# Performance work log

Measured on AMD Instinct MI355X. Metric: run time of the kernel, lower is better.

The kernel has to match this reference:

```python
import jax, jax.numpy as jnp
import numpy as np

B, T, U = 64, 512, 1024
TIME_STEP = 0.008

# Rieke cone phototransduction parameters (scaleFac = 1, values are final)
PR = dict(sigma=22.0, phi=22.0, eta=2000.0, beta=9.0, cgmp2cur=0.01,
          cgmphill=3.0, cdark=1.0, betaSlow=0.4, hillcoef=4.0,
          hillaffinity=0.5, gamma=10.0, gdark=20.0)


def setup_inputs() -> dict:
    key = jax.random.key(0)
    X = jax.random.uniform(key, (B, T, U), dtype=jnp.float32)  # light intensity >= 0
    inp = {"X_fun": X}
    for name, v in PR.items():
        inp[name] = jnp.full((1, U), v, dtype=jnp.float32)  # flax param shape (1, units)
    return inp


def reference(X_fun, sigma, phi, eta, beta, cgmp2cur, cgmphill, cdark,
              betaSlow, hillcoef, hillaffinity, gamma, gdark):
    # Derived constants (as in runRiekeModel preamble)
    darkCurrent = gdark ** cgmphill * cgmp2cur / 2
    gdark_e = (2 * darkCurrent / cgmp2cur) ** (1 / cgmphill)
    cur2ca = beta * cdark / darkCurrent
    smax = eta / phi * gdark_e * (1 + (cdark / hillaffinity) ** hillcoef)

    Bd, Td, Ud = X_fun.shape
    ones = jnp.ones((Bd, Ud), X_fun.dtype)
    g0 = gdark_e * ones
    s0 = gdark_e * eta / phi * ones
    c0 = cdark * ones
    cslow0 = cdark * ones
    r0 = X_fun[:, 0, :] * gamma / sigma
    p0 = (eta + r0) / phi

    def step(carry, x_prev):
        g, s, c, cslow, p, r = carry
        r_n = r + TIME_STEP * (-sigma * r) + gamma * x_prev
        p_n = p + TIME_STEP * (r + eta - phi * p)
        c_n = c + TIME_STEP * (cur2ca * cgmp2cur * g ** cgmphill
                               / (1 + cslow / cdark) - beta * c)
        cslow_n = cslow - TIME_STEP * (betaSlow * (cslow - c))
        s_n = smax / (1 + (c_n / hillaffinity) ** hillcoef)
        g_n = g + TIME_STEP * (s - p * g)
        return (g_n, s_n, c_n, cslow_n, p_n, r_n), g_n

    xs = jnp.moveaxis(X_fun[:, :-1, :], 1, 0)  # [T-1, B, U], step pnt uses X[:, pnt-1, :]
    _, g_seq = jax.lax.scan(step, (g0, s0, c0, cslow0, p0, r0), xs)
    # g[:, 0, :] stays zero in the original (loop starts at pnt=1)
    g = jnp.concatenate([jnp.zeros((Bd, 1, Ud), X_fun.dtype),
                         jnp.moveaxis(g_seq, 0, 1)], axis=1)
    return -(cgmp2cur * g ** cgmphill) / 2
```

## Files before the change

kernel.cpp:

```cpp
#include <hip/hip_runtime.h>
#include <math.h>


#define TT 512
#define UU 1024
#define DTSTEP 0.008f

__device__ __forceinline__ void gload16(const float* g, float* l) {
    __builtin_amdgcn_global_load_lds(
        (__attribute__((address_space(1))) void*)(uintptr_t)g,
        (__attribute__((address_space(3))) void*)l, 16, 0, 0);
}

__device__ __forceinline__ void run_fast(
    const float* __restrict__ xrow, float* __restrict__ out, unsigned ob,
    const float* gstage, float* __restrict__ wlds, int lane,
    float sigma, float phi, float eta, float beta, float cgmp2cur,
    float cdark, float betaSlow, float hillaff, float gam, float gdark)
{
    const float darkCurrent = gdark * gdark * gdark * cgmp2cur * 0.5f;
    const float gdark_e = gdark;
    const float cur2ca = beta * cdark / darkCurrent;
    const float ha2 = (cdark / hillaff) * (cdark / hillaff);
    const float smax = eta / phi * gdark_e * (1.0f + ha2 * ha2);

    const float Ar   = 1.0f - DTSTEP * sigma;
    const float P1   = 1.0f - DTSTEP * phi;
    const float Ke   = DTSTEP * eta;
    const float icd  = 1.0f / cdark;
    const float KC   = DTSTEP * cur2ca * cgmp2cur;
    const float C1   = 1.0f - DTSTEP * beta;
    const float dtbs = DTSTEP * betaSlow;
    const float iha  = 1.0f / hillaff;
    const float outk = -0.5f * cgmp2cur;

    float g  = gdark_e;
    float s  = gdark_e * eta / phi;
    float c  = cdark;
    float cs = cdark;
    float x0 = xrow[0];
    float r  = x0 * gam / sigma;
    float p  = (eta + r) / phi;
    float gp = g * g * g;

    out[ob - UU] = 0.0f;

#pragma unroll
    for (int j = 0; j < 4; ++j) {
        gload16(gstage, wlds + j * 256);
        gstage += 4 * UU;
    }

    auto step = [&](float x, float& o) {
        float rn  = fmaf(Ar, r, gam * x);
        float pn  = fmaf(P1, p, fmaf(DTSTEP, r, Ke));
        float den = fmaf(cs, icd, 1.0f);
        float rd  = __builtin_amdgcn_rcpf(den);
        float cn  = fmaf(KC, gp * rd, C1 * c);
        float csn = fmaf(-dtbs, cs - c, cs);
        float t2  = cn * iha;
        t2 *= t2;
        float sn  = smax * __builtin_amdgcn_rcpf(fmaf(t2, t2, 1.0f));
        float gn  = fmaf(DTSTEP, fmaf(-p, g, s), g);
        float gpn = gn * gn * gn;
        o = outk * gpn;
        g = gn; s = sn; c = cn; cs = csn; p = pn; r = rn; gp = gpn;
    };

    auto phase = [&](int buf, bool dostage, bool first) {
        if (first) asm volatile("s_waitcnt vmcnt(0)" ::: "memory");
        else       asm volatile("s_waitcnt vmcnt(16)" ::: "memory");
        __builtin_amdgcn_sched_barrier(0);
        if (dostage) {
#pragma unroll
            for (int j = 0; j < 4; ++j) {
                gload16(gstage, wlds + (buf ^ 1) * 1024 + j * 256);
                gstage += 4 * UU;
            }
        }
        __builtin_amdgcn_sched_barrier(0);
        const float* rb = wlds + buf * 1024 + lane;
        float xa[16];
#pragma unroll
        for (int k = 0; k < 16; ++k) xa[k] = rb[k * 64];
        __builtin_amdgcn_sched_barrier(0);
#pragma unroll
        for (int k = 0; k < 16; ++k) {
            float o;
            step(xa[k], o);
            out[ob + (unsigned)(k * UU)] = o;
        }
        ob += 16u * UU;
    };

    phase(0, true, true);
    for (int n2 = 0; n2 < 15; ++n2) {
        phase(1, true, false);
        phase(0, true, false);
    }
    asm volatile("s_waitcnt vmcnt(16)" ::: "memory");
    __builtin_amdgcn_sched_barrier(0);
    {
        const float* rb = wlds + 1024 + lane;
        float xa[16];
#pragma unroll
        for (int k = 0; k < 16; ++k) xa[k] = rb[k * 64];
#pragma unroll
        for (int k = 0; k < 15; ++k) {
            float o;
            step(xa[k], o);
            out[ob + (unsigned)(k * UU)] = o;
        }
    }
}

__device__ void run_generic(
    const float* __restrict__ xrow, float* __restrict__ out, unsigned ob,
    float sigma, float phi, float eta, float beta, float cgmp2cur,
    float cgmphill, float cdark, float betaSlow, float hillcoef,
    float hillaff, float gam, float gdark)
{
    const float darkCurrent = powf(gdark, cgmphill) * cgmp2cur * 0.5f;
    const float gdark_e = powf(2.0f * darkCurrent / cgmp2cur, 1.0f / cgmphill);
    const float cur2ca = beta * cdark / darkCurrent;
    const float smax = eta / phi * gdark_e *
                       (1.0f + powf(cdark / hillaff, hillcoef));
    float g  = gdark_e;
    float s  = gdark_e * eta / phi;
    float c  = cdark;
    float cs = cdark;
    float x0 = xrow[0];
    float r  = x0 * gam / sigma;
    float p  = (eta + r) / phi;
    out[ob - UU] = 0.0f;
    for (int t = 1; t < TT; ++t) {
        float x  = xrow[(t - 1) * UU];
        float rn = r + DTSTEP * (-sigma * r) + gam * x;
        float pn = p + DTSTEP * (r + eta - phi * p);
        float cn = c + DTSTEP * (cur2ca * cgmp2cur * powf(g, cgmphill)
                                 / (1.0f + cs / cdark) - beta * c);
        float csn = cs - DTSTEP * (betaSlow * (cs - c));
        float sn  = smax / (1.0f + powf(cn / hillaff, hillcoef));
        float gn  = g + DTSTEP * (s - p * g);
        out[ob + (unsigned)((t - 1) * UU)] =
            -(cgmp2cur * powf(gn, cgmphill)) * 0.5f;
        g = gn; s = sn; c = cn; cs = csn; p = pn; r = rn;
    }
}

__global__ __launch_bounds__(256, 1) void prfr_kernel(
    const float* __restrict__ X,
    const float* __restrict__ sigma_p, const float* __restrict__ phi_p,
    const float* __restrict__ eta_p,   const float* __restrict__ beta_p,
    const float* __restrict__ cgmp2cur_p, const float* __restrict__ cgmphill_p,
    const float* __restrict__ cdark_p, const float* __restrict__ betaSlow_p,
    const float* __restrict__ hillcoef_p, const float* __restrict__ hillaff_p,
    const float* __restrict__ gamma_p, const float* __restrict__ gdark_p,
    float* __restrict__ out, int total)
{
    __shared__ float smem[4][2][16][64];

    const int idx = blockIdx.x * blockDim.x + threadIdx.x;
    if (idx >= total) return;
    const int u = idx & (UU - 1);
    const int b = idx >> 10;
    const int w = __builtin_amdgcn_readfirstlane(threadIdx.x >> 6);
    const int lane = threadIdx.x & 63;

    const float* xrow = X + (size_t)b * (TT * UU) + u;
    const unsigned ob = (unsigned)b * (TT * UU) + UU + (unsigned)u;

    const int uq = (u - lane) + 4 * (lane & 15);
    const float* gstage = X + ((size_t)b * TT + (lane >> 4)) * UU + uq;

    const float sigma = sigma_p[u], phi = phi_p[u], eta = eta_p[u];
    const float beta = beta_p[u], cgmp2cur = cgmp2cur_p[u];
    const float cgmphill = cgmphill_p[u], cdark = cdark_p[u];
    const float betaSlow = betaSlow_p[u], hillcoef = hillcoef_p[u];
    const float hillaff = hillaff_p[u], gam = gamma_p[u], gdark = gdark_p[u];

    if (cgmphill == 3.0f && hillcoef == 4.0f) {
        run_fast(xrow, out, ob, gstage, &smem[w][0][0][0], lane,
                 sigma, phi, eta, beta, cgmp2cur, cdark, betaSlow,
                 hillaff, gam, gdark);
    } else {
        run_generic(xrow, out, ob, sigma, phi, eta, beta, cgmp2cur,
                    cgmphill, cdark, betaSlow, hillcoef, hillaff, gam, gdark);
    }
}

extern "C" void kernel_launch(void* const* d_in, const int* in_sizes, int n_in,
                              void* d_out, int out_size, void* d_ws, size_t ws_size,
                              hipStream_t stream)
{
    const float* X = (const float*)d_in[0];
    const int B = in_sizes[0] / (TT * UU);
    const int total = B * UU;
    const int block = 256;
    const int grid = (total + block - 1) / block;
    prfr_kernel<<<grid, block, 0, stream>>>(
        X,
        (const float*)d_in[1],  (const float*)d_in[2],  (const float*)d_in[3],
        (const float*)d_in[4],  (const float*)d_in[5],  (const float*)d_in[6],
        (const float*)d_in[7],  (const float*)d_in[8],  (const float*)d_in[9],
        (const float*)d_in[10], (const float*)d_in[11], (const float*)d_in[12],
        (float*)d_out, total);
}
```

Measured before the change: 255.6 us.

## Stage outputs through LDS for vectorized float4 stores with block-wide input staging

Restructures the kernel so each block covers 256 units of one batch. Input tiles are staged block-wide into a single shared buffer, and each 16-step chunk of outputs is written to LDS, then stored to global memory as coalesced float4 rows instead of scalar strided stores. The aim is to cut the number of memory transactions on the store side. In exchange it adds three block barriers per chunk and drops input double buffering, so the next load is only issued after the current tile has been read.

```diff
diff --git a/kernel.cpp b/kernel.cpp
--- a/kernel.cpp
+++ b/kernel.cpp
@@ -12,12 +12,81 @@
         (__attribute__((address_space(3))) void*)l, 16, 0, 0);
 }
 
-__device__ __forceinline__ void run_fast(
-    const float* __restrict__ xrow, float* __restrict__ out, unsigned ob,
-    const float* gstage, float* __restrict__ wlds, int lane,
+__device__ void run_generic(
+    const float* __restrict__ xrow, float* __restrict__ orow,
     float sigma, float phi, float eta, float beta, float cgmp2cur,
-    float cdark, float betaSlow, float hillaff, float gam, float gdark)
+    float cgmphill, float cdark, float betaSlow, float hillcoef,
+    float hillaff, float gam, float gdark)
 {
+    const float darkCurrent = powf(gdark, cgmphill) * cgmp2cur * 0.5f;
+    const float gdark_e = powf(2.0f * darkCurrent / cgmp2cur, 1.0f / cgmphill);
+    const float cur2ca = beta * cdark / darkCurrent;
+    const float smax = eta / phi * gdark_e *
+                       (1.0f + powf(cdark / hillaff, hillcoef));
+    float g  = gdark_e;
+    float s  = gdark_e * eta / phi;
+    float c  = cdark;
+    float cs = cdark;
+    float x0 = xrow[0];
+    float r  = x0 * gam / sigma;
+    float p  = (eta + r) / phi;
+    orow[0] = 0.0f;
+    for (int t = 1; t < TT; ++t) {
+        float x  = xrow[(t - 1) * UU];
+        float rn = r + DTSTEP * (-sigma * r) + gam * x;
+        float pn = p + DTSTEP * (r + eta - phi * p);
+        float cn = c + DTSTEP * (cur2ca * cgmp2cur * powf(g, cgmphill)
+                                 / (1.0f + cs / cdark) - beta * c);
+        float csn = cs - DTSTEP * (betaSlow * (cs - c));
+        float sn  = smax / (1.0f + powf(cn / hillaff, hillcoef));
+        float gn  = g + DTSTEP * (s - p * g);
+        orow[t * UU] = -(cgmp2cur * powf(gn, cgmphill)) * 0.5f;
+        g = gn; s = sn; c = cn; cs = csn; p = pn; r = rn;
+    }
+}
+
+__global__ __launch_bounds__(256, 1) void prfr_kernel(
+    const float* __restrict__ X,
+    const float* __restrict__ sigma_p, const float* __restrict__ phi_p,
+    const float* __restrict__ eta_p,   const float* __restrict__ beta_p,
+    const float* __restrict__ cgmp2cur_p, const float* __restrict__ cgmphill_p,
+    const float* __restrict__ cdark_p, const float* __restrict__ betaSlow_p,
+    const float* __restrict__ hillcoef_p, const float* __restrict__ hillaff_p,
+    const float* __restrict__ gamma_p, const float* __restrict__ gdark_p,
+    float* __restrict__ out, int Bn)
+{
+    __shared__ __align__(16) float SX[16][256];
+    __shared__ __align__(16) float SO[16][256];
+    __shared__ int anyslow;
+
+    const int tid  = threadIdx.x;
+    const int w    = __builtin_amdgcn_readfirstlane(tid >> 6);
+    const int lane = tid & 63;
+    const int b    = blockIdx.x >> 2;
+    const int uq   = blockIdx.x & 3;
+    const int u    = uq * 256 + tid;
+
+    const float sigma = sigma_p[u], phi = phi_p[u], eta = eta_p[u];
+    const float beta = beta_p[u], cgmp2cur = cgmp2cur_p[u];
+    const float cgmphill = cgmphill_p[u], cdark = cdark_p[u];
+    const float betaSlow = betaSlow_p[u], hillcoef = hillcoef_p[u];
+    const float hillaff = hillaff_p[u], gam = gamma_p[u], gdark = gdark_p[u];
+
+    const bool fastu = (cgmphill == 3.0f) && (hillcoef == 4.0f);
+    if (tid == 0) anyslow = 0;
+    __syncthreads();
+    if (!fastu) anyslow = 1;
+    __syncthreads();
+
+    const size_t bTU = (size_t)b * (TT * UU);
+
+    if (anyslow) {
+        run_generic(X + bTU + u, out + bTU + u, sigma, phi, eta, beta,
+                    cgmp2cur, cgmphill, cdark, betaSlow, hillcoef,
+                    hillaff, gam, gdark);
+        return;
+    }
+
     const float darkCurrent = gdark * gdark * gdark * cgmp2cur * 0.5f;
     const float gdark_e = gdark;
     const float cur2ca = beta * cdark / darkCurrent;
@@ -38,18 +107,19 @@
     float s  = gdark_e * eta / phi;
     float c  = cdark;
     float cs = cdark;
-    float x0 = xrow[0];
+    float x0 = X[bTU + u];
     float r  = x0 * gam / sigma;
     float p  = (eta + r) / phi;
     float gp = g * g * g;
 
-    out[ob - UU] = 0.0f;
+    out[bTU + u] = 0.0f;
+
+    const float* xs = X + bTU + uq * 256 + (size_t)(4 * w) * UU + lane * 4;
+    float* op = out + bTU + uq * 256 + (size_t)(w + 1) * UU + lane * 4;
 
 #pragma unroll
-    for (int j = 0; j < 4; ++j) {
-        gload16(gstage, wlds + j * 256);
-        gstage += 4 * UU;
-    }
+    for (int j = 0; j < 4; ++j) gload16(xs + j * UU, &SX[4 * w + j][0]);
+    xs += 16 * UU;
 
     auto step = [&](float x, float& o) {
         float rn  = fmaf(Ar, r, gam * x);
@@ -67,125 +137,43 @@
         g = gn; s = sn; c = cn; cs = csn; p = pn; r = rn; gp = gpn;
     };
 
-    auto phase = [&](int buf, bool dostage, bool first) {
-        if (first) asm volatile("s_waitcnt vmcnt(0)" ::: "memory");
-        else       asm volatile("s_waitcnt vmcnt(16)" ::: "memory");
+    for (int n = 0; n < 32; ++n) {
+        if (n == 0) asm volatile("s_waitcnt vmcnt(0)" ::: "memory");
+        else        asm volatile("s_waitcnt vmcnt(4)" ::: "memory");
         __builtin_amdgcn_sched_barrier(0);
-        if (dostage) {
-#pragma unroll
-            for (int j = 0; j < 4; ++j) {
-                gload16(gstage, wlds + (buf ^ 1) * 1024 + j * 256);
-                gstage += 4 * UU;
-            }
-        }
-        __builtin_amdgcn_sched_barrier(0);
-        const float* rb = wlds + buf * 1024 + lane;
+        __builtin_amdgcn_s_barrier();
+
         float xa[16];
 #pragma unroll
-        for (int k = 0; k < 16; ++k) xa[k] = rb[k * 64];
+        for (int k = 0; k < 16; ++k) xa[k] = SX[k][tid];
+        asm volatile("s_waitcnt lgkmcnt(0)" ::: "memory");
         __builtin_amdgcn_sched_barrier(0);
+        __builtin_amdgcn_s_barrier();
+
+        if (n < 31) {
+#pragma unroll
+            for (int j = 0; j < 4; ++j) gload16(xs + j * UU, &SX[4 * w + j][0]);
+            xs += 16 * UU;
+        }
+
 #pragma unroll
         for (int k = 0; k < 16; ++k) {
             float o;
             step(xa[k], o);
-            out[ob + (unsigned)(k * UU)] = o;
+            SO[k][tid] = o;
         }
-        ob += 16u * UU;
-    };
+        asm volatile("s_waitcnt lgkmcnt(0)" ::: "memory");
+        __builtin_amdgcn_sched_barrier(0);
+        __builtin_amdgcn_s_barrier();
 
-    phase(0, true, true);
-    for (int n2 = 0; n2 < 15; ++n2) {
-        phase(1, true, false);
-        phase(0, true, false);
-    }
-    asm volatile("s_waitcnt vmcnt(16)" ::: "memory");
-    __builtin_amdgcn_sched_barrier(0);
-    {
-        const float* rb = wlds + 1024 + lane;
-        float xa[16];
+        const float4* SOv = (const float4*)&SO[0][0];
 #pragma unroll
-        for (int k = 0; k < 16; ++k) xa[k] = rb[k * 64];
-#pragma unroll
-        for (int k = 0; k < 15; ++k) {
-            float o;
-            step(xa[k], o);
-            out[ob + (unsigned)(k * UU)] = o;
+        for (int j = 0; j < 4; ++j) {
+            if (n == 31 && j == 3 && w == 3) continue;
+            float4 v = SOv[j * 256 + tid];
+            *(float4*)(op + j * 4 * UU) = v;
         }
-    }
-}
-
-__device__ void run_generic(
-    const float* __restrict__ xrow, float* __restrict__ out, unsigned ob,
-    float sigma, float phi, float eta, float beta, float cgmp2cur,
-    float cgmphill, float cdark, float betaSlow, float hillcoef,
-    float hillaff, float gam, float gdark)
-{
-    const float darkCurrent = powf(gdark, cgmphill) * cgmp2cur * 0.5f;
-    const float gdark_e = powf(2.0f * darkCurrent / cgmp2cur, 1.0f / cgmphill);
-    const float cur2ca = beta * cdark / darkCurrent;
-    const float smax = eta / phi * gdark_e *
-                       (1.0f + powf(cdark / hillaff, hillcoef));
-    float g  = gdark_e;
-    float s  = gdark_e * eta / phi;
-    float c  = cdark;
-    float cs = cdark;
-    float x0 = xrow[0];
-    float r  = x0 * gam / sigma;
-    float p  = (eta + r) / phi;
-    out[ob - UU] = 0.0f;
-    for (int t = 1; t < TT; ++t) {
-        float x  = xrow[(t - 1) * UU];
-        float rn = r + DTSTEP * (-sigma * r) + gam * x;
-        float pn = p + DTSTEP * (r + eta - phi * p);
-        float cn = c + DTSTEP * (cur2ca * cgmp2cur * powf(g, cgmphill)
-                                 / (1.0f + cs / cdark) - beta * c);
-        float csn = cs - DTSTEP * (betaSlow * (cs - c));
-        float sn  = smax / (1.0f + powf(cn / hillaff, hillcoef));
-        float gn  = g + DTSTEP * (s - p * g);
-        out[ob + (unsigned)((t - 1) * UU)] =
-            -(cgmp2cur * powf(gn, cgmphill)) * 0.5f;
-        g = gn; s = sn; c = cn; cs = csn; p = pn; r = rn;
-    }
-}
-
-__global__ __launch_bounds__(256, 1) void prfr_kernel(
-    const float* __restrict__ X,
-    const float* __restrict__ sigma_p, const float* __restrict__ phi_p,
-    const float* __restrict__ eta_p,   const float* __restrict__ beta_p,
-    const float* __restrict__ cgmp2cur_p, const float* __restrict__ cgmphill_p,
-    const float* __restrict__ cdark_p, const float* __restrict__ betaSlow_p,
-    const float* __restrict__ hillcoef_p, const float* __restrict__ hillaff_p,
-    const float* __restrict__ gamma_p, const float* __restrict__ gdark_p,
-    float* __restrict__ out, int total)
-{
-    __shared__ float smem[4][2][16][64];
-
-    const int idx = blockIdx.x * blockDim.x + threadIdx.x;
-    if (idx >= total) return;
-    const int u = idx & (UU - 1);
-    const int b = idx >> 10;
-    const int w = __builtin_amdgcn_readfirstlane(threadIdx.x >> 6);
-    const int lane = threadIdx.x & 63;
-
-    const float* xrow = X + (size_t)b * (TT * UU) + u;
-    const unsigned ob = (unsigned)b * (TT * UU) + UU + (unsigned)u;
-
-    const int uq = (u - lane) + 4 * (lane & 15);
-    const float* gstage = X + ((size_t)b * TT + (lane >> 4)) * UU + uq;
-
-    const float sigma = sigma_p[u], phi = phi_p[u], eta = eta_p[u];
-    const float beta = beta_p[u], cgmp2cur = cgmp2cur_p[u];
-    const float cgmphill = cgmphill_p[u], cdark = cdark_p[u];
-    const float betaSlow = betaSlow_p[u], hillcoef = hillcoef_p[u];
-    const float hillaff = hillaff_p[u], gam = gamma_p[u], gdark = gdark_p[u];
-
-    if (cgmphill == 3.0f && hillcoef == 4.0f) {
-        run_fast(xrow, out, ob, gstage, &smem[w][0][0][0], lane,
-                 sigma, phi, eta, beta, cgmp2cur, cdark, betaSlow,
-                 hillaff, gam, gdark);
-    } else {
-        run_generic(xrow, out, ob, sigma, phi, eta, beta, cgmp2cur,
-                    cgmphill, cdark, betaSlow, hillcoef, hillaff, gam, gdark);
+        op += 16 * UU;
     }
 }
 
@@ -195,14 +183,12 @@
 {
     const float* X = (const float*)d_in[0];
     const int B = in_sizes[0] / (TT * UU);
-    const int total = B * UU;
-    const int block = 256;
-    const int grid = (total + block - 1) / block;
-    prfr_kernel<<<grid, block, 0, stream>>>(
+    const int grid = B * 4;
+    prfr_kernel<<<grid, 256, 0, stream>>>(
         X,
         (const float*)d_in[1],  (const float*)d_in[2],  (const float*)d_in[3],
         (const float*)d_in[4],  (const float*)d_in[5],  (const float*)d_in[6],
         (const float*)d_in[7],  (const float*)d_in[8],  (const float*)d_in[9],
         (const float*)d_in[10], (const float*)d_in[11], (const float*)d_in[12],
-        (float*)d_out, total);
+        (float*)d_out, B);
 }
```

After: 253.5 us. About the same (-0.8%).
